# Kernel optimization log

Measured on AMD Instinct MI355X. Metric: run time of the kernel, lower is better.

Reference implementation:

```python
import jax, jax.numpy as jnp
import numpy as np

B, N, D, DEG = 16, 8192, 384, 16
K, H, STEPS = 8, 128, 3


def setup_inputs() -> dict:
    key = jax.random.key(0)
    ks = jax.random.split(key, 8)
    s_in = 1.0 / np.sqrt(2 * D)
    s_h = 1.0 / np.sqrt(H)
    return {
        "q_embs": jax.random.normal(ks[0], (B, D), jnp.float32),
        "emb": jax.random.normal(ks[1], (B, N, D), jnp.float32),
        "neighbors": jax.random.randint(ks[2], (B, N, DEG), 0, N, jnp.int32),
        "labels": jax.random.randint(ks[3], (B, N), 0, 2, jnp.int32),
        "W1": jax.random.normal(ks[4], (2 * D, H), jnp.float32) * s_in,
        "b1": jnp.zeros((H,), jnp.float32),
        "W2": jax.random.normal(ks[5], (H, K), jnp.float32) * s_h,
        "b2": jnp.zeros((K,), jnp.float32),
        "P1": jax.random.normal(ks[6], (2 * D, H), jnp.float32) * s_in,
        "pb1": jnp.zeros((H,), jnp.float32),
        "P2": jax.random.normal(ks[7], (H, 1), jnp.float32) * s_h,
        "pb2": jnp.zeros((1,), jnp.float32),
    }


def reference(q_embs, emb, neighbors, labels, W1, b1, W2, b2, P1, pb1, P2, pb2):
    b, n, d = emb.shape
    k = W2.shape[1]
    # inp = [emb | q broadcast]  -> [B, N, 2D]
    inp = jnp.concatenate([emb, jnp.broadcast_to(q_embs[:, None, :], emb.shape)], axis=-1)
    # path_net: sigmoid(MLP) -> [B, N], then +1 at support (label==1) nodes
    path = jax.nn.sigmoid(jax.nn.relu(inp @ P1 + pb1) @ P2 + pb2)[..., 0]
    path = path + labels.astype(path.dtype)
    # coin_net amplitudes scaled by (1 + path)
    amps = (jax.nn.relu(inp @ W1 + b1) @ W2 + b2) * (1.0 + path)[..., None]  # [B,N,K]
    # initial uniform state
    state = jnp.full((b, n, k), 1.0 / np.sqrt(n * k), dtype=emb.dtype)

    # sparse adjacency diffusion: out[i] = sum_{j in nbrs[i]} st[j]
    spmm = jax.vmap(lambda st, nb: st[nb].sum(axis=1))  # st [N,K], nb [N,DEG]

    for _ in range(STEPS):
        st = spmm(state * amps, neighbors)                 # [B,N,K]
        norm = jnp.linalg.norm(st.reshape(b, -1), axis=1)[:, None, None]
        state = jnp.where(norm > 0, st / norm, st)
    return jnp.abs(state).sum(axis=-1)  # [B,N]
```

## Files before the change

### kernel.cpp

```cpp
#include <hip/hip_runtime.h>
#include <cstdint>
#include <cstddef>

#define BB 16
#define NN 8192
#define DD 384
#define HH 128
#define KK 8
#define DEG 16

typedef short bf8_t __attribute__((ext_vector_type(8)));
typedef float f4_t __attribute__((ext_vector_type(4)));

typedef const __attribute__((address_space(1))) unsigned char* gcp_t;
typedef __attribute__((address_space(3))) unsigned char* lcp_t;

__device__ __forceinline__ void glds16(const void* g, void* l) {
  __builtin_amdgcn_global_load_lds((gcp_t)g, (lcp_t)l, 16, 0, 0);
}

__device__ __forceinline__ unsigned short f2bf(float f) {
  unsigned int u = __float_as_uint(f);
  u += 0x7FFFu + ((u >> 16) & 1u);
  return (unsigned short)(u >> 16);
}

__device__ __forceinline__ bf8_t pack8(float4 f0, float4 f1) {
  union { unsigned short us[8]; bf8_t v; } pk;
  pk.us[0] = f2bf(f0.x); pk.us[1] = f2bf(f0.y);
  pk.us[2] = f2bf(f0.z); pk.us[3] = f2bf(f0.w);
  pk.us[4] = f2bf(f1.x); pk.us[5] = f2bf(f1.y);
  pk.us[6] = f2bf(f1.z); pk.us[7] = f2bf(f1.w);
  return pk.v;
}

__global__ __launch_bounds__(256) void kprep(
    const float* __restrict__ q, const float* __restrict__ W1,
    const float* __restrict__ b1, const float* __restrict__ P1,
    const float* __restrict__ pb1,
    unsigned short* __restrict__ W1t, unsigned short* __restrict__ P1t,
    float* __restrict__ base1, float* __restrict__ baseP,
    float* __restrict__ normsq)
{
  int blk = blockIdx.x, t = threadIdx.x;
  if (blk < 32) {
    int b = blk >> 1, net = blk & 1;
    const float* W = (net ? P1 : W1) + (size_t)DD * HH;
    const float* qb = q + b * DD;
    int h = t & 127, half = t >> 7;
    int d0 = half * 192;
    float a0 = 0.f, a1 = 0.f, a2 = 0.f, a3 = 0.f;
    for (int d = d0; d < d0 + 192; d += 4) {
      a0 = fmaf(qb[d],     W[(size_t)d * HH + h],       a0);
      a1 = fmaf(qb[d + 1], W[(size_t)(d + 1) * HH + h], a1);
      a2 = fmaf(qb[d + 2], W[(size_t)(d + 2) * HH + h], a2);
      a3 = fmaf(qb[d + 3], W[(size_t)(d + 3) * HH + h], a3);
    }
    __shared__ float red[256];
    red[t] = (a0 + a1) + (a2 + a3);
    __syncthreads();
    if (t < 128) {
      float tot = red[t] + red[t + 128] + (net ? pb1[h] : b1[h]);
      (net ? baseP : base1)[b * HH + h] = tot;
    }
  } else {
    int e = (blk - 32) * 3072 + t;
    for (int it = 0; it < 12; ++it, e += 256) {
      int net = e / 49152;
      int r = e - net * 49152;
      int d = r >> 7;
      int h = r & 127;
      float v = (net ? P1 : W1)[d * HH + h];
      int ph = d >> 6;
      int rem = d & 63;
      int cb = rem >> 3, wi = rem & 7;
      int c = cb ^ (h & 7);
      (net ? P1t : W1t)[ph * 8192 + h * 64 + c * 8 + wi] = f2bf(v);
    }
    if (blk == 32 && t < BB) normsq[t] = 0.f;
  }
}

__global__ __launch_bounds__(512, 4) void kgemm(
    const float* __restrict__ emb,
    const unsigned short* __restrict__ W1t, const unsigned short* __restrict__ P1t,
    const float* __restrict__ base1, const float* __restrict__ baseP,
    const float* __restrict__ W2, const float* __restrict__ b2,
    const float* __restrict__ P2, const float* __restrict__ pb2,
    float* __restrict__ rawamps, float* __restrict__ pslogit)
{
  __shared__ __align__(16) unsigned short sB[2][128 * 64];
  __shared__ float sW2a[128 * 9];
  __shared__ float sBase[128];
  __shared__ float sP2[128];
  __shared__ float sB2[8];

  const int g = blockIdx.x;
  const int slot = g & 7;
  const int net = (g >> 3) & 1;
  const int wid = (g >> 4) * 8 + slot;
  const int b = wid >> 5;
  const int rowbase = (wid & 31) * 256;

  const int t = threadIdx.x;
  const int w = t >> 6, lane = t & 63, q = lane >> 4, ln = lane & 15;
  const int fl = ln & 7;

  const unsigned short* Wsw = net ? P1t : W1t;

  {
    const unsigned short* src = Wsw + w * 512 + lane * 8;
    char* dst = (char*)&sB[0][0] + w * 1024;
    glds16(src,        dst);
    glds16(src + 4096, dst + 8192);
  }
  if (t < 128) sBase[t] = (net ? baseP : base1)[b * HH + t];
  if (net == 0) {
    for (int e = t; e < HH * KK; e += 512) {
      int h = e >> 3, kk = e & 7;
      sW2a[h * 9 + kk] = W2[e];
    }
    if (t < 8) sB2[t] = b2[t];
  } else if (t >= 128 && t < 256) {
    sP2[t - 128] = P2[t - 128];
  }

  const float* ar0 = emb + (size_t)(b * NN + rowbase + w * 32 + ln) * DD + q * 8;
  const float* ar1 = ar0 + (size_t)16 * DD;
  float4 pf[4];
  pf[0] = ((const float4*)ar0)[0]; pf[1] = ((const float4*)ar0)[1];
  pf[2] = ((const float4*)ar1)[0]; pf[3] = ((const float4*)ar1)[1];

  f4_t acc[2][8];
  f4_t zero = {0.f, 0.f, 0.f, 0.f};
#pragma unroll
  for (int i = 0; i < 8; ++i) { acc[0][i] = zero; acc[1][i] = zero; }

  __syncthreads();

#pragma unroll
  for (int ph = 0; ph < 6; ++ph) {
    if (ph < 5) {
      const unsigned short* src = Wsw + (ph + 1) * 8192 + w * 512 + lane * 8;
      char* dst = (char*)&sB[0][0] + ((ph + 1) & 1) * 16384 + w * 1024;
      glds16(src,        dst);
      glds16(src + 4096, dst + 8192);
    }
    const char* bbase = (const char*)&sB[0][0] + (ph & 1) * 16384;
#pragma unroll
    for (int jl = 0; jl < 2; ++jl) {
      const int j = ph * 2 + jl;
      bf8_t af0 = pack8(pf[0], pf[1]);
      bf8_t af1 = pack8(pf[2], pf[3]);
      if (j + 1 < 12) {
        const float* p0 = ar0 + (j + 1) * 32;
        const float* p1 = ar1 + (j + 1) * 32;
        pf[0] = ((const float4*)p0)[0]; pf[1] = ((const float4*)p0)[1];
        pf[2] = ((const float4*)p1)[0]; pf[3] = ((const float4*)p1)[1];
      }
      const int cb = jl * 4 + q;
#pragma unroll
      for (int ct = 0; ct < 8; ++ct) {
        const int h = ct * 16 + ln;
        bf8_t bf = *(const bf8_t*)(bbase + h * 128 + ((cb ^ fl) << 4));
        acc[0][ct] = __builtin_amdgcn_mfma_f32_16x16x32_bf16(af0, bf, acc[0][ct], 0, 0, 0);
        acc[1][ct] = __builtin_amdgcn_mfma_f32_16x16x32_bf16(af1, bf, acc[1][ct], 0, 0, 0);
      }
    }
    if (ph < 5) __syncthreads();
  }

  const float pb2v = pb2[0];
#pragma unroll
  for (int grp = 0; grp < 2; ++grp) {
#pragma unroll
    for (int r = 0; r < 4; ++r) {
      const int grow = rowbase + w * 32 + grp * 16 + q * 4 + r;
      if (net == 0) {
        float s[8];
#pragma unroll
        for (int kk = 0; kk < 8; ++kk) s[kk] = 0.f;
#pragma unroll
        for (int ct = 0; ct < 8; ++ct) {
          int col = ct * 16 + ln;
          float h1 = fmaxf(acc[grp][ct][r] + sBase[col], 0.f);
#pragma unroll
          for (int kk = 0; kk < 8; ++kk) s[kk] = fmaf(h1, sW2a[col * 9 + kk], s[kk]);
        }
#pragma unroll
        for (int off = 1; off < 16; off <<= 1)
#pragma unroll
          for (int kk = 0; kk < 8; ++kk) s[kk] += __shfl_xor(s[kk], off, 64);
        if (ln == 0) {
          float4 o0, o1;
          o0.x = s[0] + sB2[0]; o0.y = s[1] + sB2[1];
          o0.z = s[2] + sB2[2]; o0.w = s[3] + sB2[3];
          o1.x = s[4] + sB2[4]; o1.y = s[5] + sB2[5];
          o1.z = s[6] + sB2[6]; o1.w = s[7] + sB2[7];
          float4* dst = (float4*)(rawamps + (size_t)(b * NN + grow) * KK);
          dst[0] = o0; dst[1] = o1;
        }
      } else {
        float ps = 0.f;
#pragma unroll
        for (int ct = 0; ct < 8; ++ct) {
          int col = ct * 16 + ln;
          float hp = fmaxf(acc[grp][ct][r] + sBase[col], 0.f);
          ps = fmaf(hp, sP2[col], ps);
        }
#pragma unroll
        for (int off = 1; off < 16; off <<= 1) ps += __shfl_xor(ps, off, 64);
        if (ln == 0) pslogit[b * NN + grow] = ps + pb2v;
      }
    }
  }
}

__global__ __launch_bounds__(256) void applyscale(
    const float* __restrict__ raw, const float* __restrict__ psl,
    const int* __restrict__ lab, float* __restrict__ ampsP)
{
  int node = blockIdx.x * 256 + threadIdx.x;
  float sc = 1.f + 1.f / (1.f + __expf(-psl[node])) + (float)lab[node];
  const float4* r = (const float4*)(raw + (size_t)node * KK);
  float4 v0 = r[0], v1 = r[1];
  const int BN = BB * NN;
  ampsP[0 * BN + node] = v0.x * sc;
  ampsP[1 * BN + node] = v0.y * sc;
  ampsP[2 * BN + node] = v0.z * sc;
  ampsP[3 * BN + node] = v0.w * sc;
  ampsP[4 * BN + node] = v1.x * sc;
  ampsP[5 * BN + node] = v1.y * sc;
  ampsP[6 * BN + node] = v1.z * sc;
  ampsP[7 * BN + node] = v1.w * sc;
}

__global__ __launch_bounds__(1024, 4) void sdiff(
    const int* __restrict__ nbr, const float* __restrict__ ampsP,
    float* __restrict__ u3P, float* __restrict__ normsq)
{
  __shared__ float sAmp[NN];
  __shared__ float sSt[NN];
  const int g = blockIdx.x;
  const int b = g & 15;
  const int k = g >> 4;
  const int t = threadIdx.x;
  const int BN = BB * NN;

  {
    const float4* p4 = (const float4*)(ampsP + (size_t)k * BN + (size_t)b * NN);
    float4* s4 = (float4*)sAmp;
    s4[t] = p4[t];
    s4[t + 1024] = p4[t + 1024];
  }

  const int* nbase = nbr + (size_t)b * NN * DEG;
  int4 qv[8][4];
#pragma unroll
  for (int i = 0; i < 8; ++i) {
    const int4* np = (const int4*)(nbase + (size_t)(i * 1024 + t) * DEG);
    qv[i][0] = np[0]; qv[i][1] = np[1]; qv[i][2] = np[2]; qv[i][3] = np[3];
  }
  __syncthreads();

  float res[8];

#define GSTEP(SRC)                                                         \
  _Pragma("unroll")                                                        \
  for (int i = 0; i < 8; ++i) {                                            \
    float a = SRC[qv[i][0].x] + SRC[qv[i][0].y]                            \
            + SRC[qv[i][0].z] + SRC[qv[i][0].w]                            \
            + SRC[qv[i][1].x] + SRC[qv[i][1].y]                            \
            + SRC[qv[i][1].z] + SRC[qv[i][1].w]                            \
            + SRC[qv[i][2].x] + SRC[qv[i][2].y]                            \
            + SRC[qv[i][2].z] + SRC[qv[i][2].w]                            \
            + SRC[qv[i][3].x] + SRC[qv[i][3].y]                            \
            + SRC[qv[i][3].z] + SRC[qv[i][3].w];                           \
    res[i] = a;                                                            \
  }

  GSTEP(sAmp)
#pragma unroll
  for (int i = 0; i < 8; ++i) sSt[i * 1024 + t] = res[i] * sAmp[i * 1024 + t];
  __syncthreads();

  GSTEP(sSt)
  __syncthreads();
#pragma unroll
  for (int i = 0; i < 8; ++i) sSt[i * 1024 + t] = res[i] * sAmp[i * 1024 + t];
  __syncthreads();

  GSTEP(sSt)
#undef GSTEP
  float* oplane = u3P + (size_t)k * BN + (size_t)b * NN;
  float ss = 0.f;
#pragma unroll
  for (int i = 0; i < 8; ++i) {
    oplane[i * 1024 + t] = res[i];
    ss = fmaf(res[i], res[i], ss);
  }
#pragma unroll
  for (int o = 1; o < 64; o <<= 1) ss += __shfl_xor(ss, o, 64);
  if ((t & 63) == 0) atomicAdd(&normsq[b], ss);
}

__global__ __launch_bounds__(256) void fout(
    const float* __restrict__ u3P, const float* __restrict__ normsq,
    float* __restrict__ out)
{
  int node = blockIdx.x * 256 + threadIdx.x;
  float ns = normsq[node >> 13];
  float inv = ns > 0.f ? rsqrtf(ns) : 1.f;
  const int BN = BB * NN;
  float s = fabsf(u3P[0 * BN + node]) + fabsf(u3P[1 * BN + node])
          + fabsf(u3P[2 * BN + node]) + fabsf(u3P[3 * BN + node])
          + fabsf(u3P[4 * BN + node]) + fabsf(u3P[5 * BN + node])
          + fabsf(u3P[6 * BN + node]) + fabsf(u3P[7 * BN + node]);
  out[node] = s * inv;
}

extern "C" void kernel_launch(void* const* d_in, const int* in_sizes, int n_in,
                              void* d_out, int out_size, void* d_ws, size_t ws_size,
                              hipStream_t stream) {
  const float* q   = (const float*)d_in[0];
  const float* emb = (const float*)d_in[1];
  const int*   nbr = (const int*)d_in[2];
  const int*   lab = (const int*)d_in[3];
  const float* W1  = (const float*)d_in[4];
  const float* b1  = (const float*)d_in[5];
  const float* W2  = (const float*)d_in[6];
  const float* b2  = (const float*)d_in[7];
  const float* P1  = (const float*)d_in[8];
  const float* pb1 = (const float*)d_in[9];
  const float* P2  = (const float*)d_in[10];
  const float* pb2 = (const float*)d_in[11];
  float* out = (float*)d_out;

  const size_t NK = (size_t)BB * NN * KK;
  float* ws     = (float*)d_ws;
  float* buf0   = ws;
  float* buf1   = buf0 + NK;
  float* buf2   = buf1 + NK;
  float* psl    = buf2 + NK;
  float* base1  = psl + (size_t)BB * NN;
  float* baseP  = base1 + BB * HH;
  float* normsq = baseP + BB * HH;
  unsigned short* W1t = (unsigned short*)(normsq + 16);
  unsigned short* P1t = W1t + (size_t)HH * DD;

  kprep<<<64, 256, 0, stream>>>(q, W1, b1, P1, pb1, W1t, P1t, base1, baseP, normsq);
  kgemm<<<1024, 512, 0, stream>>>(emb, W1t, P1t, base1, baseP, W2, b2, P2, pb2,
                                  buf0, psl);
  applyscale<<<512, 256, 0, stream>>>(buf0, psl, lab, buf1);
  sdiff<<<128, 1024, 0, stream>>>(nbr, buf1, buf2, normsq);
  fout<<<512, 256, 0, stream>>>(buf2, normsq, out);
}
```

Measured before the change: 409.0 us.

## Fuse amplitude scaling into diffusion kernel and pipeline GEMM LDS loads with setprio

Removes the separate applyscale kernel: sdiff now computes the sigmoid path scale and multiplies the raw coin amplitudes while loading them into shared memory, reading strided raw values directly. This drops one launch and a round trip of the transposed amplitude buffer. The GEMM main loop also swaps __syncthreads for an explicit vmcnt(2) wait plus s_barrier so the prefetched LDS tile can stay in flight, and raises wave priority around the MFMA block. In exchange, the strided raw loads in sdiff are less coalesced and every k-block recomputes the exp, and the manual waitcnt depends on the exact count of outstanding loads.

```diff
diff --git a/kernel.cpp b/kernel.cpp
--- a/kernel.cpp
+++ b/kernel.cpp
@@ -146,6 +146,9 @@
       glds16(src,        dst);
       glds16(src + 4096, dst + 8192);
     }
+    asm volatile("s_waitcnt vmcnt(2)" ::: "memory");
+    __builtin_amdgcn_s_barrier();
+
     const char* bbase = (const char*)&sB[0][0] + (ph & 1) * 16384;
 #pragma unroll
     for (int jl = 0; jl < 2; ++jl) {
@@ -159,6 +162,7 @@
         pf[2] = ((const float4*)p1)[0]; pf[3] = ((const float4*)p1)[1];
       }
       const int cb = jl * 4 + q;
+      __builtin_amdgcn_s_setprio(1);
 #pragma unroll
       for (int ct = 0; ct < 8; ++ct) {
         const int h = ct * 16 + ln;
@@ -166,8 +170,9 @@
         acc[0][ct] = __builtin_amdgcn_mfma_f32_16x16x32_bf16(af0, bf, acc[0][ct], 0, 0, 0);
         acc[1][ct] = __builtin_amdgcn_mfma_f32_16x16x32_bf16(af1, bf, acc[1][ct], 0, 0, 0);
       }
-    }
-    if (ph < 5) __syncthreads();
+      __builtin_amdgcn_s_setprio(0);
+    }
+    if (ph < 5) __builtin_amdgcn_s_barrier();
   }
 
   const float pb2v = pb2[0];
@@ -216,27 +221,9 @@
   }
 }
 
-__global__ __launch_bounds__(256) void applyscale(
-    const float* __restrict__ raw, const float* __restrict__ psl,
-    const int* __restrict__ lab, float* __restrict__ ampsP)
-{
-  int node = blockIdx.x * 256 + threadIdx.x;
-  float sc = 1.f + 1.f / (1.f + __expf(-psl[node])) + (float)lab[node];
-  const float4* r = (const float4*)(raw + (size_t)node * KK);
-  float4 v0 = r[0], v1 = r[1];
-  const int BN = BB * NN;
-  ampsP[0 * BN + node] = v0.x * sc;
-  ampsP[1 * BN + node] = v0.y * sc;
-  ampsP[2 * BN + node] = v0.z * sc;
-  ampsP[3 * BN + node] = v0.w * sc;
-  ampsP[4 * BN + node] = v1.x * sc;
-  ampsP[5 * BN + node] = v1.y * sc;
-  ampsP[6 * BN + node] = v1.z * sc;
-  ampsP[7 * BN + node] = v1.w * sc;
-}
-
 __global__ __launch_bounds__(1024, 4) void sdiff(
-    const int* __restrict__ nbr, const float* __restrict__ ampsP,
+    const int* __restrict__ nbr, const float* __restrict__ raw,
+    const float* __restrict__ psl, const int* __restrict__ lab,
     float* __restrict__ u3P, float* __restrict__ normsq)
 {
   __shared__ float sAmp[NN];
@@ -247,11 +234,14 @@
   const int t = threadIdx.x;
   const int BN = BB * NN;
 
-  {
-    const float4* p4 = (const float4*)(ampsP + (size_t)k * BN + (size_t)b * NN);
-    float4* s4 = (float4*)sAmp;
-    s4[t] = p4[t];
-    s4[t + 1024] = p4[t + 1024];
+  const float* rawb = raw + ((size_t)b * NN) * KK + k;
+  const float* pslb = psl + (size_t)b * NN;
+  const int*   labb = lab + (size_t)b * NN;
+#pragma unroll
+  for (int i = 0; i < 8; ++i) {
+    int n = i * 1024 + t;
+    float sc = 1.f + 1.f / (1.f + __expf(-pslb[n])) + (float)labb[n];
+    sAmp[n] = rawb[(size_t)n * KK] * sc;
   }
 
   const int* nbase = nbr + (size_t)b * NN * DEG;
@@ -351,7 +341,6 @@
   kprep<<<64, 256, 0, stream>>>(q, W1, b1, P1, pb1, W1t, P1t, base1, baseP, normsq);
   kgemm<<<1024, 512, 0, stream>>>(emb, W1t, P1t, base1, baseP, W2, b2, P2, pb2,
                                   buf0, psl);
-  applyscale<<<512, 256, 0, stream>>>(buf0, psl, lab, buf1);
-  sdiff<<<128, 1024, 0, stream>>>(nbr, buf1, buf2, normsq);
+  sdiff<<<128, 1024, 0, stream>>>(nbr, buf0, psl, lab, buf2, normsq);
   fout<<<512, 256, 0, stream>>>(buf2, normsq, out);
 }
```

Result: no change. 412.2 us (+0.8%).
